# Performance work log

Hardware: AMD Instinct MI355X
Metric: run time of the kernel (lower is better)

The kernel has to match this reference:

```python
import jax, jax.numpy as jnp
import numpy as np

N_P, N_D = 100000, 50000
C, S, H = 128, 128, 128
E = 600000


def setup_inputs() -> dict:
    key = jax.random.key(0)
    ks = jax.random.split(key, 20)
    sc = 1.0 / np.sqrt(H)
    inp = {
        "h_p": jax.random.normal(ks[0], (N_P, C), dtype=jnp.float32),
        "h_d": jax.random.normal(ks[1], (N_D, S), dtype=jnp.float32),
        "pd_src": jax.random.randint(ks[2], (E,), 0, N_P),
        "pd_dst": jax.random.randint(ks[3], (E,), 0, N_D),
        "dp_src": jax.random.randint(ks[4], (E,), 0, N_D),
        "dp_dst": jax.random.randint(ks[5], (E,), 0, N_P),
    }
    names = [("W1_pd", (C, H)), ("W1_dp", (S, H)), ("W2_pd", (H, H)),
             ("W2_dp", (H, H)), ("W3_pd", (H, S)), ("W3_dp", (H, C))]
    for i, (nm, shp) in enumerate(names):
        inp[nm] = jax.random.normal(ks[6 + i], shp, dtype=jnp.float32) * sc
        inp["b" + nm[1:]] = jnp.zeros((shp[1],), dtype=jnp.float32)
    return inp


def gconv(x, src, dst, n_dst, W, b):
    """DGL GraphConv, norm='both': relu(D_dst^-1/2 A D_src^-1/2 X W + b)."""
    n_src = x.shape[0]
    ones = jnp.ones(src.shape, dtype=x.dtype)
    deg_out = jnp.maximum(jax.ops.segment_sum(ones, src, num_segments=n_src), 1.0)
    deg_in = jnp.maximum(jax.ops.segment_sum(ones, dst, num_segments=n_dst), 1.0)
    xs = x * jax.lax.rsqrt(deg_out)[:, None]
    m = jax.ops.segment_sum(xs[src], dst, num_segments=n_dst)  # [n_dst, d_in]
    m = m * jax.lax.rsqrt(deg_in)[:, None]
    return jax.nn.relu(m @ W + b)


def reference(h_p, h_d, pd_src, pd_dst, dp_src, dp_dst,
              W1_pd, b1_pd, W1_dp, b1_dp,
              W2_pd, b2_pd, W2_dp, b2_dp,
              W3_pd, b3_pd, W3_dp, b3_dp):
    # Layer 1: p_d sends p feats to d; d_p sends d feats to p
    h_d1 = gconv(h_p, pd_src, pd_dst, N_D, W1_pd, b1_pd)
    h_p1 = gconv(h_d, dp_src, dp_dst, N_P, W1_dp, b1_dp)
    # Layer 2
    h_d2 = gconv(h_p1, pd_src, pd_dst, N_D, W2_pd, b2_pd)
    h_p2 = gconv(h_d1, dp_src, dp_dst, N_P, W2_dp, b2_dp)
    # Layer 3: d gets S-dim, p gets C-dim
    h_d3 = gconv(h_p2, pd_src, pd_dst, N_D, W3_pd, b3_pd)
    h_p3 = gconv(h_d2, dp_src, dp_dst, N_P, W3_dp, b3_dp)
    return h_p3, h_d3
```

## Files before the change

kernel.cpp:

```cpp
#include <hip/hip_runtime.h>
#include <stdint.h>

#define N_P 100000
#define N_D 50000
#define NE  600000
#define F   128
#define FP  136

#define NCHK   16
#define CHKE   37504
#define HPH    4
#define HPS    8
#define HOFS_A0 ((size_t)0)
#define HOFS_A1 ((size_t)NCHK*N_P)
#define HOFS_A2 ((size_t)NCHK*N_P + (size_t)NCHK*N_D)
#define HOFS_A3 ((size_t)NCHK*N_P + (size_t)2*NCHK*N_D)

typedef __attribute__((ext_vector_type(8))) __bf16 bf16x8;
typedef __attribute__((ext_vector_type(4))) float  f32x4;

static __device__ __forceinline__ float bf2f(uint16_t u){
  union{float f;uint32_t i;} v; v.i = ((uint32_t)u)<<16; return v.f;
}
static __device__ __forceinline__ uint16_t f2bf(float f){
  union{float f;uint32_t i;} v; v.f = f;
  uint32_t i = v.i;
  uint32_t r = i + 0x7fffu + ((i>>16)&1u);
  return (uint16_t)(r>>16);
}

__global__ __launch_bounds__(512) void k_hist(
    const int* __restrict__ pd_src, const int* __restrict__ pd_dst,
    const int* __restrict__ dp_src, const int* __restrict__ dp_dst,
    int* __restrict__ hist){
  __shared__ uint32_t cnt[(N_P/HPH)/2];
  const int b = blockIdx.x;
  const int arr = b >> 6, part = (b >> 4) & 3, chunk = b & 15;
  const int* src; int N; size_t hofs;
  switch(arr){
    case 0:  src = pd_src; N = N_P; hofs = HOFS_A0; break;
    case 1:  src = pd_dst; N = N_D; hofs = HOFS_A1; break;
    case 2:  src = dp_src; N = N_D; hofs = HOFS_A2; break;
    default: src = dp_dst; N = N_P; hofs = HOFS_A3; break;
  }
  const int PART = N / HPH;
  const int nw   = PART >> 1;
  const int lo   = part * PART;
  for (int i = threadIdx.x; i < nw; i += 512) cnt[i] = 0;
  __syncthreads();
  const int e0 = chunk*CHKE, e1 = min(e0 + CHKE, NE);
  const uint4* s4 = (const uint4*)(src + e0);
  const int n4 = (e1 - e0) >> 2;
  for (int i = threadIdx.x; i < n4; i += 512){
    uint4 v = s4[i];
    int a0 = (int)v.x - lo, a1 = (int)v.y - lo, a2 = (int)v.z - lo, a3 = (int)v.w - lo;
    if ((unsigned)a0 < (unsigned)PART) atomicAdd(&cnt[a0>>1], 1u << ((a0&1)<<4));
    if ((unsigned)a1 < (unsigned)PART) atomicAdd(&cnt[a1>>1], 1u << ((a1&1)<<4));
    if ((unsigned)a2 < (unsigned)PART) atomicAdd(&cnt[a2>>1], 1u << ((a2&1)<<4));
    if ((unsigned)a3 < (unsigned)PART) atomicAdd(&cnt[a3>>1], 1u << ((a3&1)<<4));
  }
  __syncthreads();
  int* out = hist + hofs + (size_t)chunk*N + lo;
  for (int i = threadIdx.x; i < nw; i += 512){
    uint32_t w = cnt[i];
    out[2*i]   = (int)(w & 0xffffu);
    out[2*i+1] = (int)(w >> 16);
  }
}

__global__ void k_sumdeg(int* __restrict__ hist,
                         int* __restrict__ cnt_d_in, int* __restrict__ cnt_p_in,
                         float* __restrict__ rs_p_out, float* __restrict__ rs_p_in,
                         float* __restrict__ rs_d_out, float* __restrict__ rs_d_in){
  const int idx = blockIdx.x*256 + threadIdx.x;
  const int arr = blockIdx.y;
  int N; size_t hofs; bool pre;
  switch(arr){
    case 0:  N = N_P; hofs = HOFS_A0; pre = false; break;
    case 1:  N = N_D; hofs = HOFS_A1; pre = true;  break;
    case 2:  N = N_D; hofs = HOFS_A2; pre = false; break;
    default: N = N_P; hofs = HOFS_A3; pre = true;  break;
  }
  if (idx >= N) return;
  int* base = hist + hofs + idx;
  int run = 0;
  if (pre){
    #pragma unroll 4
    for (int c = 0; c < NCHK; ++c){
      int v = base[(size_t)c*N]; base[(size_t)c*N] = run; run += v;
    }
  } else {
    #pragma unroll 4
    for (int c = 0; c < NCHK; ++c) run += base[(size_t)c*N];
  }
  float rs = rsqrtf((float)max(run, 1));
  switch(arr){
    case 0:  rs_p_out[idx] = rs; break;
    case 1:  cnt_d_in[idx] = run; rs_d_in[idx] = rs; break;
    case 2:  rs_d_out[idx] = rs; break;
    default: cnt_p_in[idx] = run; rs_p_in[idx] = rs; break;
  }
}

__global__ void k_scan1(const int* __restrict__ cA, int nA,
                        const int* __restrict__ cB, int nB,
                        int* __restrict__ bsums, int nbA){
  __shared__ int red[8];
  int b = blockIdx.x, t = threadIdx.x;
  const int* in; int n, bi, slot;
  if (b < nbA){ in = cA; n = nA; bi = b;       slot = bi; }
  else        { in = cB; n = nB; bi = b - nbA; slot = 256 + bi; }
  int i = bi*512 + t;
  int v = (i < n) ? in[i] : 0;
  #pragma unroll
  for (int o = 32; o; o >>= 1) v += __shfl_down(v, o, 64);
  if ((t & 63) == 0) red[t >> 6] = v;
  __syncthreads();
  if (t == 0){ int s = 0; for (int k = 0; k < 8; ++k) s += red[k]; bsums[slot] = s; }
}

__global__ void k_scan2(int* bsums, int nbA, int nbB){
  __shared__ int sh[256];
  int seg = blockIdx.x, t = threadIdx.x;
  int nb = seg ? nbB : nbA;
  int* p = bsums + seg*256;
  int v = (t < nb) ? p[t] : 0;
  sh[t] = v; __syncthreads();
  for (int ofs = 1; ofs < 256; ofs <<= 1){
    int u = (t >= ofs) ? sh[t-ofs] : 0; __syncthreads();
    sh[t] += u; __syncthreads();
  }
  if (t < nb) p[t] = sh[t] - v;
}

__global__ void k_scan3(const int* __restrict__ cA, int nA,
                        const int* __restrict__ cB, int nB,
                        const int* __restrict__ bsums, int nbA,
                        int* __restrict__ offA, int* __restrict__ offB){
  __shared__ int sh[512];
  int b = blockIdx.x, t = threadIdx.x;
  const int* in; int n, bi; int* out; int base;
  if (b < nbA){ in = cA; n = nA; bi = b;       out = offA; base = bsums[bi]; }
  else        { in = cB; n = nB; bi = b - nbA; out = offB; base = bsums[256+bi]; }
  int i = bi*512 + t;
  int v = (i < n) ? in[i] : 0;
  sh[t] = v; __syncthreads();
  for (int ofs = 1; ofs < 512; ofs <<= 1){
    int u = (t >= ofs) ? sh[t-ofs] : 0; __syncthreads();
    sh[t] += u; __syncthreads();
  }
  if (i < n) out[i] = base + sh[t] - v;
  if (b == 0 && t == 0){ offA[nA] = NE; offB[nB] = NE; }
}

__global__ __launch_bounds__(512) void k_scatter(
    const int* __restrict__ pd_src, const int* __restrict__ pd_dst,
    const int* __restrict__ dp_src, const int* __restrict__ dp_dst,
    const int* __restrict__ off_pd, const int* __restrict__ off_dp,
    const int* __restrict__ hist,
    int* __restrict__ col_pd, int* __restrict__ col_dp){
  __shared__ int base[N_P/HPS];
  const int b = blockIdx.x;
  const int gph = b >> 7, part = (b >> 4) & 7, chunk = b & 15;
  const int* dsts; const int* srcs; const int* off; int* col; int N; size_t hofs;
  if (gph == 0){ dsts = pd_dst; srcs = pd_src; off = off_pd; col = col_pd; N = N_D; hofs = HOFS_A1; }
  else         { dsts = dp_dst; srcs = dp_src; off = off_dp; col = col_dp; N = N_P; hofs = HOFS_A3; }
  const int PART = N / HPS;
  const int lo = part * PART;
  const int* hc   = hist + hofs + (size_t)chunk*N + lo;
  const int* offp = off + lo;
  for (int i = threadIdx.x; i < PART; i += 512) base[i] = offp[i] + hc[i];
  __syncthreads();
  const int e0 = chunk*CHKE, e1 = min(e0 + CHKE, NE);
  const uint4* d4 = (const uint4*)(dsts + e0);
  const int n4 = (e1 - e0) >> 2;
  for (int i = threadIdx.x; i < n4; i += 512){
    uint4 d = d4[i];
    int a0 = (int)d.x - lo, a1 = (int)d.y - lo, a2 = (int)d.z - lo, a3 = (int)d.w - lo;
    int e = e0 + 4*i;
    if ((unsigned)a0 < (unsigned)PART){ int p = atomicAdd(&base[a0], 1); col[p] = srcs[e+0]; }
    if ((unsigned)a1 < (unsigned)PART){ int p = atomicAdd(&base[a1], 1); col[p] = srcs[e+1]; }
    if ((unsigned)a2 < (unsigned)PART){ int p = atomicAdd(&base[a2], 1); col[p] = srcs[e+2]; }
    if ((unsigned)a3 < (unsigned)PART){ int p = atomicAdd(&base[a3], 1); col[p] = srcs[e+3]; }
  }
}

__global__ void k_convert(const float4* __restrict__ hp, const float4* __restrict__ hd,
                          const float* __restrict__ rs_po, const float* __restrict__ rs_do,
                          uint2* __restrict__ P0, uint2* __restrict__ D0,
                          const float* w0,const float* w1,const float* w2,
                          const float* w3,const float* w4,const float* w5,
                          uint16_t* __restrict__ wt,
                          uint16_t* z0, uint16_t* z1, uint16_t* z2,
                          uint16_t* z3, uint16_t* z4, uint16_t* z5){
  if (blockIdx.x < 6){
    int m = blockIdx.x;
    const float* W; uint16_t* Z;
    switch(m){ case 0:W=w0;Z=z0;break; case 1:W=w1;Z=z1;break; case 2:W=w2;Z=z2;break;
               case 3:W=w3;Z=z3;break; case 4:W=w4;Z=z4;break; default:W=w5;Z=z5; }
    uint16_t* T = wt + m*F*FP;
    for (int idx = threadIdx.x; idx < F*F; idx += 256){
      int k = idx >> 7, j = idx & 127;
      T[j*FP + k] = f2bf(W[idx]);
    }
    if (threadIdx.x < F) Z[threadIdx.x] = 0;
    return;
  }
  int i = (blockIdx.x - 6)*256 + threadIdx.x;
  const int nP4 = N_P*F/4, nD4 = N_D*F/4;
  if (i < nP4){
    float4 v = hp[i]; float s = rs_po[i >> 5];
    uint2 r;
    r.x = ((uint32_t)f2bf(v.y*s)<<16) | f2bf(v.x*s);
    r.y = ((uint32_t)f2bf(v.w*s)<<16) | f2bf(v.z*s);
    P0[i] = r;
  } else {
    int j = i - nP4;
    if (j < nD4){
      float4 v = hd[j]; float s = rs_do[j >> 5];
      uint2 r;
      r.x = ((uint32_t)f2bf(v.y*s)<<16) | f2bf(v.x*s);
      r.y = ((uint32_t)f2bf(v.w*s)<<16) | f2bf(v.z*s);
      D0[j] = r;
    }
  }
}

template<int OUT_MODE>
__global__ __launch_bounds__(256, 4) void k_gconv2(
    const uint16_t* __restrict__ xA, const int* __restrict__ offAp, const int* __restrict__ colA,
    const float* __restrict__ rsA, const uint16_t* __restrict__ WtA, const float* __restrict__ biasA,
    const float* __restrict__ rsnA, void* __restrict__ outA, int ndA, int nsA, int nblkA,
    const uint16_t* __restrict__ xB, const int* __restrict__ offBp, const int* __restrict__ colB,
    const float* __restrict__ rsB, const uint16_t* __restrict__ WtB, const float* __restrict__ biasB,
    const float* __restrict__ rsnB, void* __restrict__ outB, int ndB, int nsB)
{
  __shared__ uint16_t m_lds[64*FP];
  const int tid  = threadIdx.x;
  const int lane = tid & 63;
  const int wv   = tid >> 6;

  const uint16_t* x; const int* off; const int* col; const float* rs_in;
  const uint16_t* Wt; const float* bias; const float* rs_next; void* outp;
  int n_dst, zrow, bid;
  if ((int)blockIdx.x < nblkA){
    x = xA; off = offAp; col = colA; rs_in = rsA; Wt = WtA; bias = biasA;
    rs_next = rsnA; outp = outA; n_dst = ndA; zrow = nsA; bid = blockIdx.x;
  } else {
    x = xB; off = offBp; col = colB; rs_in = rsB; Wt = WtB; bias = biasB;
    rs_next = rsnB; outp = outB; n_dst = ndB; zrow = nsB; bid = blockIdx.x - nblkA;
  }

  const int row0 = bid*64 + wv*16;
  const int g    = lane >> 4;
  const int l    = lane & 15;
  const uint16_t* xl = x + l*8;

  int e0a[4], e1a[4], cva[4];
  #pragma unroll
  for (int i = 0; i < 4; ++i){
    int r = row0 + i*4 + g;
    bool rv = r < n_dst;
    e0a[i] = rv ? off[r]   : 0;
    e1a[i] = rv ? off[r+1] : 0;
  }
  #pragma unroll
  for (int i = 0; i < 4; ++i){
    int last = (e1a[i] > 0) ? e1a[i]-1 : 0;
    int idx  = e0a[i] + l;
    cva[i] = col[idx < e1a[i] ? idx : last];
  }

  #pragma unroll
  for (int i = 0; i < 4; ++i){
    int e0 = e0a[i], e1 = e1a[i];
    int cv = cva[i];
    float a0=0.f,a1=0.f,a2=0.f,a3=0.f,a4=0.f,a5=0.f,a6=0.f,a7=0.f;
    for (int e = e0; e < e1; e += 16){
      int nidx = e + 16 + l;
      int ncv  = col[nidx < e1 ? nidx : e1-1];
      int cnt  = e1 - e;
      const bool more = (cnt > 8);
      int cb[16];
      #pragma unroll
      for (int q = 0; q < 8; ++q) cb[q] = __shfl(cv, g*16 + q, 64);
      if (more){
        #pragma unroll
        for (int q = 8; q < 16; ++q) cb[q] = __shfl(cv, g*16 + q, 64);
      }
      uint4 u[8], w[8];
      #pragma unroll
      for (int q = 0; q < 8; ++q){
        int c = (q < cnt) ? cb[q] : zrow;
        u[q] = *(const uint4*)(xl + (size_t)c*F);
      }
      if (more){
        #pragma unroll
        for (int q = 8; q < 16; ++q){
          int c = (q < cnt) ? cb[q] : zrow;
          w[q-8] = *(const uint4*)(xl + (size_t)c*F);
        }
      }
      #pragma unroll
      for (int q = 0; q < 8; ++q){
        a0 += bf2f((uint16_t)u[q].x); a1 += bf2f((uint16_t)(u[q].x>>16));
        a2 += bf2f((uint16_t)u[q].y); a3 += bf2f((uint16_t)(u[q].y>>16));
        a4 += bf2f((uint16_t)u[q].z); a5 += bf2f((uint16_t)(u[q].z>>16));
        a6 += bf2f((uint16_t)u[q].w); a7 += bf2f((uint16_t)(u[q].w>>16));
      }
      if (more){
        #pragma unroll
        for (int q = 0; q < 8; ++q){
          a0 += bf2f((uint16_t)w[q].x); a1 += bf2f((uint16_t)(w[q].x>>16));
          a2 += bf2f((uint16_t)w[q].y); a3 += bf2f((uint16_t)(w[q].y>>16));
          a4 += bf2f((uint16_t)w[q].z); a5 += bf2f((uint16_t)(w[q].z>>16));
          a6 += bf2f((uint16_t)w[q].w); a7 += bf2f((uint16_t)(w[q].w>>16));
        }
      }
      cv = ncv;
    }
    int r = row0 + i*4 + g;
    float rs = (r < n_dst) ? rs_in[r] : 0.f;
    uint4 pk;
    pk.x = ((uint32_t)f2bf(a1*rs)<<16) | f2bf(a0*rs);
    pk.y = ((uint32_t)f2bf(a3*rs)<<16) | f2bf(a2*rs);
    pk.z = ((uint32_t)f2bf(a5*rs)<<16) | f2bf(a4*rs);
    pk.w = ((uint32_t)f2bf(a7*rs)<<16) | f2bf(a6*rs);
    *(uint4*)&m_lds[(wv*16 + i*4 + g)*FP + l*8] = pk;
  }

  f32x4 acc[8];
  #pragma unroll
  for (int t = 0; t < 8; ++t) acc[t] = (f32x4){0.f,0.f,0.f,0.f};
  const int mrow = lane & 15;
  const int kgrp = lane >> 4;
  #pragma unroll
  for (int k0 = 0; k0 < F; k0 += 32){
    bf16x8 bfrag = *(const bf16x8*)&m_lds[(wv*16 + mrow)*FP + k0 + kgrp*8];
    #pragma unroll
    for (int t = 0; t < 8; ++t){
      bf16x8 afrag = *(const bf16x8*)&Wt[(t*16 + mrow)*FP + k0 + kgrp*8];
      acc[t] = __builtin_amdgcn_mfma_f32_16x16x32_bf16(afrag, bfrag, acc[t], 0, 0, 0);
    }
  }

  const int q4 = kgrp * 4;
  const int rr = row0 + mrow;
  if (rr < n_dst){
    float rsn = (OUT_MODE == 0) ? rs_next[rr] : 1.f;
    #pragma unroll
    for (int t = 0; t < 8; ++t){
      float4 b4 = *(const float4*)&bias[t*16 + q4];
      float v0 = fmaxf(acc[t][0] + b4.x, 0.f);
      float v1 = fmaxf(acc[t][1] + b4.y, 0.f);
      float v2 = fmaxf(acc[t][2] + b4.z, 0.f);
      float v3 = fmaxf(acc[t][3] + b4.w, 0.f);
      if (OUT_MODE == 0){
        uint2 pk;
        pk.x = ((uint32_t)f2bf(v1*rsn)<<16) | f2bf(v0*rsn);
        pk.y = ((uint32_t)f2bf(v3*rsn)<<16) | f2bf(v2*rsn);
        *(uint2*)((uint16_t*)outp + (size_t)rr*F + t*16 + q4) = pk;
      } else {
        float4 o; o.x = v0; o.y = v1; o.z = v2; o.w = v3;
        *(float4*)((float*)outp + (size_t)rr*F + t*16 + q4) = o;
      }
    }
  }
}

extern "C" void kernel_launch(void* const* d_in, const int* in_sizes, int n_in,
                              void* d_out, int out_size, void* d_ws, size_t ws_size,
                              hipStream_t stream) {
  const float* h_p   = (const float*)d_in[0];
  const float* h_d   = (const float*)d_in[1];
  const int* pd_src  = (const int*)d_in[2];
  const int* pd_dst  = (const int*)d_in[3];
  const int* dp_src  = (const int*)d_in[4];
  const int* dp_dst  = (const int*)d_in[5];
  const float* W1_pd = (const float*)d_in[6];   const float* b1_pd = (const float*)d_in[7];
  const float* W1_dp = (const float*)d_in[8];   const float* b1_dp = (const float*)d_in[9];
  const float* W2_pd = (const float*)d_in[10];  const float* b2_pd = (const float*)d_in[11];
  const float* W2_dp = (const float*)d_in[12];  const float* b2_dp = (const float*)d_in[13];
  const float* W3_pd = (const float*)d_in[14];  const float* b3_pd = (const float*)d_in[15];
  const float* W3_dp = (const float*)d_in[16];  const float* b3_dp = (const float*)d_in[17];

  char* w = (char*)d_ws;
  size_t o = 0;
  auto take = [&](size_t bytes)->char*{
    char* p = w + o; o += (bytes + 255) & ~(size_t)255; return p;
  };

  int* cnt_d_in  = (int*)take(4*(size_t)N_D);
  int* cnt_p_in  = (int*)take(4*(size_t)N_P);
  int* off_pd   = (int*)take(4*(size_t)(N_D+1));
  int* off_dp   = (int*)take(4*(size_t)(N_P+1));
  int* bsums    = (int*)take(4*512);
  int* col_pd   = (int*)take(4*(size_t)NE);
  int* col_dp   = (int*)take(4*(size_t)NE);
  float* rs_p_out = (float*)take(4*(size_t)N_P);
  float* rs_p_in  = (float*)take(4*(size_t)N_P);
  float* rs_d_out = (float*)take(4*(size_t)N_D);
  float* rs_d_in  = (float*)take(4*(size_t)N_D);
  uint16_t* wt  = (uint16_t*)take(2*(size_t)6*F*FP);
  uint16_t* P0  = (uint16_t*)take(2*(size_t)(N_P+1)*F);
  uint16_t* P1  = (uint16_t*)take(2*(size_t)(N_P+1)*F);
  uint16_t* P2  = (uint16_t*)take(2*(size_t)(N_P+1)*F);
  uint16_t* D0  = (uint16_t*)take(2*(size_t)(N_D+1)*F);
  uint16_t* D1  = (uint16_t*)take(2*(size_t)(N_D+1)*F);
  uint16_t* D2  = (uint16_t*)take(2*(size_t)(N_D+1)*F);

  int* hist = (int*)P1;

  k_hist<<<4*HPH*NCHK, 512, 0, stream>>>(pd_src, pd_dst, dp_src, dp_dst, hist);
  k_sumdeg<<<dim3((N_P+255)/256, 4), 256, 0, stream>>>(
      hist, cnt_d_in, cnt_p_in, rs_p_out, rs_p_in, rs_d_out, rs_d_in);
  const int nbA = (N_D + 511)/512;
  const int nbB = (N_P + 511)/512;
  k_scan1<<<nbA+nbB, 512, 0, stream>>>(cnt_d_in, N_D, cnt_p_in, N_P, bsums, nbA);
  k_scan2<<<2, 256, 0, stream>>>(bsums, nbA, nbB);
  k_scan3<<<nbA+nbB, 512, 0, stream>>>(cnt_d_in, N_D, cnt_p_in, N_P, bsums, nbA, off_pd, off_dp);
  k_scatter<<<2*HPS*NCHK, 512, 0, stream>>>(pd_src, pd_dst, dp_src, dp_dst,
                                            off_pd, off_dp, hist, col_pd, col_dp);
  k_convert<<<((N_P+N_D)*F/4 + 255)/256 + 6, 256, 0, stream>>>(
      (const float4*)h_p, (const float4*)h_d, rs_p_out, rs_d_out, (uint2*)P0, (uint2*)D0,
      W1_pd, W1_dp, W2_pd, W2_dp, W3_pd, W3_dp, wt,
      P0 + (size_t)N_P*F, D0 + (size_t)N_D*F,
      P1 + (size_t)N_P*F, D1 + (size_t)N_D*F,
      P2 + (size_t)N_P*F, D2 + (size_t)N_D*F);

  const int gd = (N_D + 63)/64, gp = (N_P + 63)/64;
  k_gconv2<0><<<gd+gp, 256, 0, stream>>>(
      P0, off_pd, col_pd, rs_d_in, wt + 0*F*FP, b1_pd, rs_d_out, D1, N_D, N_P, gd,
      D0, off_dp, col_dp, rs_p_in, wt + 1*F*FP, b1_dp, rs_p_out, P1, N_P, N_D);
  k_gconv2<0><<<gd+gp, 256, 0, stream>>>(
      P1, off_pd, col_pd, rs_d_in, wt + 2*F*FP, b2_pd, rs_d_out, D2, N_D, N_P, gd,
      D1, off_dp, col_dp, rs_p_in, wt + 3*F*FP, b2_dp, rs_p_out, P2, N_P, N_D);
  k_gconv2<1><<<gd+gp, 256, 0, stream>>>(
      P2, off_pd, col_pd, rs_d_in, wt + 4*F*FP, b3_pd, nullptr, (float*)d_out + (size_t)N_P*F, N_D, N_P, gd,
      D2, off_dp, col_dp, rs_p_in, wt + 5*F*FP, b3_dp, nullptr, (float*)d_out, N_P, N_D);
}
```

Baseline: 446.9 us.

## Fuse CSR build and feature conversion into one cooperative kernel with grid syncs

Replaces the seven preprocessing launches (histogram, degree sum, three-phase scan, scatter, convert) with a single cooperative kernel of 256 blocks that separates the phases with grid.sync(). The feature/weight conversion work is spread into the phases that are otherwise underutilised, such as the scan stages, so it overlaps with them. Launch gaps and tail idle time between the small kernels are meant to be removed. The gather loads in the aggregation kernel also switch to nontemporal loads. Risks: grid-sync cost, a fixed grid of 256 blocks for the histogram and scatter phases, and a fallback path if the cooperative launch fails.

```diff
diff --git a/kernel.cpp b/kernel.cpp
--- a/kernel.cpp
+++ b/kernel.cpp
@@ -1,5 +1,8 @@
 #include <hip/hip_runtime.h>
+#include <hip/hip_cooperative_groups.h>
 #include <stdint.h>
+
+namespace cg = cooperative_groups;
 
 #define N_P 100000
 #define N_D 50000
@@ -11,13 +14,20 @@
 #define CHKE   37504
 #define HPH    4
 #define HPS    8
+#define NBLD   256
+#define NBA    ((N_D + 511)/512)
+#define NBB    ((N_P + 511)/512)
 #define HOFS_A0 ((size_t)0)
 #define HOFS_A1 ((size_t)NCHK*N_P)
 #define HOFS_A2 ((size_t)NCHK*N_P + (size_t)NCHK*N_D)
 #define HOFS_A3 ((size_t)NCHK*N_P + (size_t)2*NCHK*N_D)
+#define CVT_TOT (6 + (N_P+N_D)*F/4/256)
+#define CVT_A   6252
+#define CVT_B   12504
 
 typedef __attribute__((ext_vector_type(8))) __bf16 bf16x8;
 typedef __attribute__((ext_vector_type(4))) float  f32x4;
+typedef unsigned int __attribute__((ext_vector_type(4))) u32x4;
 
 static __device__ __forceinline__ float bf2f(uint16_t u){
   union{float f;uint32_t i;} v; v.i = ((uint32_t)u)<<16; return v.f;
@@ -27,6 +37,256 @@
   uint32_t i = v.i;
   uint32_t r = i + 0x7fffu + ((i>>16)&1u);
   return (uint16_t)(r>>16);
+}
+static __device__ __forceinline__ uint4 ld_nt_u4(const uint16_t* p){
+  u32x4 v = __builtin_nontemporal_load((const u32x4*)p);
+  uint4 r; r.x = v.x; r.y = v.y; r.z = v.z; r.w = v.w; return r;
+}
+
+static __device__ __forceinline__ void convert_ob(
+    int ob, int t,
+    const float4* __restrict__ hp, const float4* __restrict__ hd,
+    const float* __restrict__ rs_po, const float* __restrict__ rs_do,
+    uint2* __restrict__ P0, uint2* __restrict__ D0,
+    const float* w0,const float* w1,const float* w2,
+    const float* w3,const float* w4,const float* w5,
+    uint16_t* __restrict__ wt,
+    uint16_t* z0, uint16_t* z1, uint16_t* z2,
+    uint16_t* z3, uint16_t* z4, uint16_t* z5)
+{
+  if (ob < 6){
+    const float* W; uint16_t* Z;
+    switch(ob){ case 0:W=w0;Z=z0;break; case 1:W=w1;Z=z1;break; case 2:W=w2;Z=z2;break;
+                case 3:W=w3;Z=z3;break; case 4:W=w4;Z=z4;break; default:W=w5;Z=z5; }
+    uint16_t* T = wt + ob*F*FP;
+    for (int idx = t; idx < F*F; idx += 256){
+      int k = idx >> 7, j = idx & 127;
+      T[j*FP + k] = f2bf(W[idx]);
+    }
+    if (t < F) Z[t] = 0;
+    return;
+  }
+  int i = (ob - 6)*256 + t;
+  const int nP4 = N_P*F/4, nD4 = N_D*F/4;
+  if (i < nP4){
+    float4 v = hp[i]; float s = rs_po[i >> 5];
+    uint2 r;
+    r.x = ((uint32_t)f2bf(v.y*s)<<16) | f2bf(v.x*s);
+    r.y = ((uint32_t)f2bf(v.w*s)<<16) | f2bf(v.z*s);
+    P0[i] = r;
+  } else {
+    int j = i - nP4;
+    if (j < nD4){
+      float4 v = hd[j]; float s = rs_do[j >> 5];
+      uint2 r;
+      r.x = ((uint32_t)f2bf(v.y*s)<<16) | f2bf(v.x*s);
+      r.y = ((uint32_t)f2bf(v.w*s)<<16) | f2bf(v.z*s);
+      D0[j] = r;
+    }
+  }
+}
+
+__global__ __launch_bounds__(512) void k_build(
+    const int* __restrict__ pd_src, const int* __restrict__ pd_dst,
+    const int* __restrict__ dp_src, const int* __restrict__ dp_dst,
+    int* __restrict__ hist,
+    int* __restrict__ cnt_d_in, int* __restrict__ cnt_p_in,
+    float* __restrict__ rs_p_out, float* __restrict__ rs_p_in,
+    float* __restrict__ rs_d_out, float* __restrict__ rs_d_in,
+    int* __restrict__ bsums,
+    int* __restrict__ off_pd, int* __restrict__ off_dp,
+    int* __restrict__ col_pd, int* __restrict__ col_dp,
+    const float4* __restrict__ hp, const float4* __restrict__ hd,
+    uint2* __restrict__ P0, uint2* __restrict__ D0,
+    const float* w0,const float* w1,const float* w2,
+    const float* w3,const float* w4,const float* w5,
+    uint16_t* __restrict__ wt,
+    uint16_t* z0, uint16_t* z1, uint16_t* z2,
+    uint16_t* z3, uint16_t* z4, uint16_t* z5)
+{
+  __shared__ union {
+    uint32_t cnt[(N_P/HPH)/2];
+    int      base[N_P/HPS];
+    int      sh512[512];
+    int      sh256[256];
+  } sm;
+  __shared__ int red2[8];
+  cg::grid_group grid = cg::this_grid();
+  const int t = threadIdx.x;
+  const int b = blockIdx.x;
+
+  {
+    const int arr = b >> 6, part = (b >> 4) & 3, chunk = b & 15;
+    const int* src; int N; size_t hofs;
+    switch(arr){
+      case 0:  src = pd_src; N = N_P; hofs = HOFS_A0; break;
+      case 1:  src = pd_dst; N = N_D; hofs = HOFS_A1; break;
+      case 2:  src = dp_src; N = N_D; hofs = HOFS_A2; break;
+      default: src = dp_dst; N = N_P; hofs = HOFS_A3; break;
+    }
+    const int PART = N / HPH;
+    const int nw   = PART >> 1;
+    const int lo   = part * PART;
+    for (int i = t; i < nw; i += 512) sm.cnt[i] = 0;
+    __syncthreads();
+    const int e0 = chunk*CHKE, e1 = min(e0 + CHKE, NE);
+    const uint4* s4 = (const uint4*)(src + e0);
+    const int n4 = (e1 - e0) >> 2;
+    for (int i = t; i < n4; i += 512){
+      uint4 v = s4[i];
+      int a0 = (int)v.x - lo, a1 = (int)v.y - lo, a2 = (int)v.z - lo, a3 = (int)v.w - lo;
+      if ((unsigned)a0 < (unsigned)PART) atomicAdd(&sm.cnt[a0>>1], 1u << ((a0&1)<<4));
+      if ((unsigned)a1 < (unsigned)PART) atomicAdd(&sm.cnt[a1>>1], 1u << ((a1&1)<<4));
+      if ((unsigned)a2 < (unsigned)PART) atomicAdd(&sm.cnt[a2>>1], 1u << ((a2&1)<<4));
+      if ((unsigned)a3 < (unsigned)PART) atomicAdd(&sm.cnt[a3>>1], 1u << ((a3&1)<<4));
+    }
+    __syncthreads();
+    int* out = hist + hofs + (size_t)chunk*N + lo;
+    for (int i = t; i < nw; i += 512){
+      uint32_t wv = sm.cnt[i];
+      out[2*i]   = (int)(wv & 0xffffu);
+      out[2*i+1] = (int)(wv >> 16);
+    }
+  }
+  grid.sync();
+
+  {
+    const int gtid = b*512 + t;
+    const int T0 = N_P, T1 = N_P+N_D, T2 = N_P+2*N_D, T3 = 2*N_P+2*N_D;
+    for (int w = gtid; w < T3; w += NBLD*512){
+      int arr, idx;
+      if      (w < T0){ arr = 0; idx = w; }
+      else if (w < T1){ arr = 1; idx = w - T0; }
+      else if (w < T2){ arr = 2; idx = w - T1; }
+      else            { arr = 3; idx = w - T2; }
+      int N; size_t hofs; bool pre;
+      switch(arr){
+        case 0:  N = N_P; hofs = HOFS_A0; pre = false; break;
+        case 1:  N = N_D; hofs = HOFS_A1; pre = true;  break;
+        case 2:  N = N_D; hofs = HOFS_A2; pre = false; break;
+        default: N = N_P; hofs = HOFS_A3; pre = true;  break;
+      }
+      int* basep = hist + hofs + idx;
+      int run = 0;
+      if (pre){
+        #pragma unroll 4
+        for (int c = 0; c < NCHK; ++c){
+          int v = basep[(size_t)c*N]; basep[(size_t)c*N] = run; run += v;
+        }
+      } else {
+        #pragma unroll 4
+        for (int c = 0; c < NCHK; ++c) run += basep[(size_t)c*N];
+      }
+      float rs = rsqrtf((float)max(run, 1));
+      switch(arr){
+        case 0:  rs_p_out[idx] = rs; break;
+        case 1:  cnt_d_in[idx] = run; rs_d_in[idx] = rs; break;
+        case 2:  rs_d_out[idx] = rs; break;
+        default: cnt_p_in[idx] = run; rs_p_in[idx] = rs; break;
+      }
+    }
+  }
+  grid.sync();
+
+  {
+    for (int tb = b; tb < NBA+NBB; tb += NBLD){
+      const int* in; int n, bi, slot;
+      if (tb < NBA){ in = cnt_d_in; n = N_D; bi = tb;       slot = bi; }
+      else         { in = cnt_p_in; n = N_P; bi = tb - NBA; slot = 256 + bi; }
+      int i = bi*512 + t;
+      int v = (i < n) ? in[i] : 0;
+      #pragma unroll
+      for (int o = 32; o; o >>= 1) v += __shfl_down(v, o, 64);
+      if ((t & 63) == 0) red2[t >> 6] = v;
+      __syncthreads();
+      if (t == 0){ int s = 0; for (int k = 0; k < 8; ++k) s += red2[k]; bsums[slot] = s; }
+      __syncthreads();
+    }
+    for (int p0 = 0 + b*2; p0 < CVT_A; p0 += NBLD*2){
+      int ob = p0 + (t >> 8);
+      if (ob < CVT_A)
+        convert_ob(ob, t & 255, hp, hd, rs_p_out, rs_d_out, P0, D0,
+                   w0,w1,w2,w3,w4,w5, wt, z0,z1,z2,z3,z4,z5);
+    }
+  }
+  grid.sync();
+
+  if (b == 0){
+    for (int seg = 0; seg < 2; ++seg){
+      int nb = seg ? NBB : NBA;
+      int* p = bsums + seg*256;
+      int v = 0;
+      if (t < 256){ v = (t < nb) ? p[t] : 0; sm.sh256[t] = v; }
+      __syncthreads();
+      for (int ofs = 1; ofs < 256; ofs <<= 1){
+        int u2 = 0;
+        if (t < 256 && t >= ofs) u2 = sm.sh256[t-ofs];
+        __syncthreads();
+        if (t < 256) sm.sh256[t] += u2;
+        __syncthreads();
+      }
+      if (t < nb) p[t] = sm.sh256[t] - v;
+      __syncthreads();
+    }
+  } else {
+    for (int p0 = CVT_A + (b-1)*2; p0 < CVT_B; p0 += (NBLD-1)*2){
+      int ob = p0 + (t >> 8);
+      if (ob < CVT_B)
+        convert_ob(ob, t & 255, hp, hd, rs_p_out, rs_d_out, P0, D0,
+                   w0,w1,w2,w3,w4,w5, wt, z0,z1,z2,z3,z4,z5);
+    }
+  }
+  grid.sync();
+
+  {
+    for (int tb = b; tb < NBA+NBB; tb += NBLD){
+      const int* in; int n, bi; int* outp; int base;
+      if (tb < NBA){ in = cnt_d_in; n = N_D; bi = tb;       outp = off_pd; base = bsums[bi]; }
+      else         { in = cnt_p_in; n = N_P; bi = tb - NBA; outp = off_dp; base = bsums[256+bi]; }
+      int i = bi*512 + t;
+      int v = (i < n) ? in[i] : 0;
+      sm.sh512[t] = v; __syncthreads();
+      for (int ofs = 1; ofs < 512; ofs <<= 1){
+        int u2 = (t >= ofs) ? sm.sh512[t-ofs] : 0; __syncthreads();
+        sm.sh512[t] += u2; __syncthreads();
+      }
+      if (i < n) outp[i] = base + sm.sh512[t] - v;
+      __syncthreads();
+    }
+    if (b == 0 && t == 0){ off_pd[N_D] = NE; off_dp[N_P] = NE; }
+    for (int p0 = CVT_B + b*2; p0 < CVT_TOT; p0 += NBLD*2){
+      int ob = p0 + (t >> 8);
+      if (ob < CVT_TOT)
+        convert_ob(ob, t & 255, hp, hd, rs_p_out, rs_d_out, P0, D0,
+                   w0,w1,w2,w3,w4,w5, wt, z0,z1,z2,z3,z4,z5);
+    }
+  }
+  grid.sync();
+
+  {
+    const int gph = b >> 7, part = (b >> 4) & 7, chunk = b & 15;
+    const int* dsts; const int* srcs; const int* off; int* col; int N; size_t hofs;
+    if (gph == 0){ dsts = pd_dst; srcs = pd_src; off = off_pd; col = col_pd; N = N_D; hofs = HOFS_A1; }
+    else         { dsts = dp_dst; srcs = dp_src; off = off_dp; col = col_dp; N = N_P; hofs = HOFS_A3; }
+    const int PART = N / HPS;
+    const int lo = part * PART;
+    const int* hc   = hist + hofs + (size_t)chunk*N + lo;
+    const int* offp = off + lo;
+    for (int i = t; i < PART; i += 512) sm.base[i] = offp[i] + hc[i];
+    __syncthreads();
+    const int e0 = chunk*CHKE, e1 = min(e0 + CHKE, NE);
+    const uint4* d4 = (const uint4*)(dsts + e0);
+    const int n4 = (e1 - e0) >> 2;
+    for (int i = t; i < n4; i += 512){
+      uint4 d = d4[i];
+      int a0 = (int)d.x - lo, a1 = (int)d.y - lo, a2 = (int)d.z - lo, a3 = (int)d.w - lo;
+      int e = e0 + 4*i;
+      if ((unsigned)a0 < (unsigned)PART){ int p = atomicAdd(&sm.base[a0], 1); col[p] = srcs[e+0]; }
+      if ((unsigned)a1 < (unsigned)PART){ int p = atomicAdd(&sm.base[a1], 1); col[p] = srcs[e+1]; }
+      if ((unsigned)a2 < (unsigned)PART){ int p = atomicAdd(&sm.base[a2], 1); col[p] = srcs[e+2]; }
+      if ((unsigned)a3 < (unsigned)PART){ int p = atomicAdd(&sm.base[a3], 1); col[p] = srcs[e+3]; }
+    }
+  }
 }
 
 __global__ __launch_bounds__(512) void k_hist(
@@ -193,37 +453,8 @@
                           uint16_t* __restrict__ wt,
                           uint16_t* z0, uint16_t* z1, uint16_t* z2,
                           uint16_t* z3, uint16_t* z4, uint16_t* z5){
-  if (blockIdx.x < 6){
-    int m = blockIdx.x;
-    const float* W; uint16_t* Z;
-    switch(m){ case 0:W=w0;Z=z0;break; case 1:W=w1;Z=z1;break; case 2:W=w2;Z=z2;break;
-               case 3:W=w3;Z=z3;break; case 4:W=w4;Z=z4;break; default:W=w5;Z=z5; }
-    uint16_t* T = wt + m*F*FP;
-    for (int idx = threadIdx.x; idx < F*F; idx += 256){
-      int k = idx >> 7, j = idx & 127;
-      T[j*FP + k] = f2bf(W[idx]);
-    }
-    if (threadIdx.x < F) Z[threadIdx.x] = 0;
-    return;
-  }
-  int i = (blockIdx.x - 6)*256 + threadIdx.x;
-  const int nP4 = N_P*F/4, nD4 = N_D*F/4;
-  if (i < nP4){
-    float4 v = hp[i]; float s = rs_po[i >> 5];
-    uint2 r;
-    r.x = ((uint32_t)f2bf(v.y*s)<<16) | f2bf(v.x*s);
-    r.y = ((uint32_t)f2bf(v.w*s)<<16) | f2bf(v.z*s);
-    P0[i] = r;
-  } else {
-    int j = i - nP4;
-    if (j < nD4){
-      float4 v = hd[j]; float s = rs_do[j >> 5];
-      uint2 r;
-      r.x = ((uint32_t)f2bf(v.y*s)<<16) | f2bf(v.x*s);
-      r.y = ((uint32_t)f2bf(v.w*s)<<16) | f2bf(v.z*s);
-      D0[j] = r;
-    }
-  }
+  convert_ob(blockIdx.x, threadIdx.x, hp, hd, rs_po, rs_do, P0, D0,
+             w0,w1,w2,w3,w4,w5, wt, z0,z1,z2,z3,z4,z5);
 }
 
 template<int OUT_MODE>
@@ -292,13 +523,13 @@
       #pragma unroll
       for (int q = 0; q < 8; ++q){
         int c = (q < cnt) ? cb[q] : zrow;
-        u[q] = *(const uint4*)(xl + (size_t)c*F);
+        u[q] = ld_nt_u4(xl + (size_t)c*F);
       }
       if (more){
         #pragma unroll
         for (int q = 8; q < 16; ++q){
           int c = (q < cnt) ? cb[q] : zrow;
-          w[q-8] = *(const uint4*)(xl + (size_t)c*F);
+          w[q-8] = ld_nt_u4(xl + (size_t)c*F);
         }
       }
       #pragma unroll
@@ -411,22 +642,44 @@
 
   int* hist = (int*)P1;
 
-  k_hist<<<4*HPH*NCHK, 512, 0, stream>>>(pd_src, pd_dst, dp_src, dp_dst, hist);
-  k_sumdeg<<<dim3((N_P+255)/256, 4), 256, 0, stream>>>(
-      hist, cnt_d_in, cnt_p_in, rs_p_out, rs_p_in, rs_d_out, rs_d_in);
-  const int nbA = (N_D + 511)/512;
-  const int nbB = (N_P + 511)/512;
-  k_scan1<<<nbA+nbB, 512, 0, stream>>>(cnt_d_in, N_D, cnt_p_in, N_P, bsums, nbA);
-  k_scan2<<<2, 256, 0, stream>>>(bsums, nbA, nbB);
-  k_scan3<<<nbA+nbB, 512, 0, stream>>>(cnt_d_in, N_D, cnt_p_in, N_P, bsums, nbA, off_pd, off_dp);
-  k_scatter<<<2*HPS*NCHK, 512, 0, stream>>>(pd_src, pd_dst, dp_src, dp_dst,
-                                            off_pd, off_dp, hist, col_pd, col_dp);
-  k_convert<<<((N_P+N_D)*F/4 + 255)/256 + 6, 256, 0, stream>>>(
-      (const float4*)h_p, (const float4*)h_d, rs_p_out, rs_d_out, (uint2*)P0, (uint2*)D0,
-      W1_pd, W1_dp, W2_pd, W2_dp, W3_pd, W3_dp, wt,
-      P0 + (size_t)N_P*F, D0 + (size_t)N_D*F,
-      P1 + (size_t)N_P*F, D1 + (size_t)N_D*F,
-      P2 + (size_t)N_P*F, D2 + (size_t)N_D*F);
+  const float4* hp4 = (const float4*)h_p;
+  const float4* hd4 = (const float4*)h_d;
+  uint2* P0u = (uint2*)P0;
+  uint2* D0u = (uint2*)D0;
+  uint16_t* z0 = P0 + (size_t)N_P*F;
+  uint16_t* z1 = D0 + (size_t)N_D*F;
+  uint16_t* z2 = P1 + (size_t)N_P*F;
+  uint16_t* z3 = D1 + (size_t)N_D*F;
+  uint16_t* z4 = P2 + (size_t)N_P*F;
+  uint16_t* z5 = D2 + (size_t)N_D*F;
+
+  void* kargs[] = {
+    (void*)&pd_src, (void*)&pd_dst, (void*)&dp_src, (void*)&dp_dst,
+    (void*)&hist, (void*)&cnt_d_in, (void*)&cnt_p_in,
+    (void*)&rs_p_out, (void*)&rs_p_in, (void*)&rs_d_out, (void*)&rs_d_in,
+    (void*)&bsums, (void*)&off_pd, (void*)&off_dp, (void*)&col_pd, (void*)&col_dp,
+    (void*)&hp4, (void*)&hd4, (void*)&P0u, (void*)&D0u,
+    (void*)&W1_pd, (void*)&W1_dp, (void*)&W2_pd, (void*)&W2_dp, (void*)&W3_pd, (void*)&W3_dp,
+    (void*)&wt,
+    (void*)&z0, (void*)&z1, (void*)&z2, (void*)&z3, (void*)&z4, (void*)&z5
+  };
+  hipError_t cerr = hipLaunchCooperativeKernel(reinterpret_cast<void*>(k_build),
+                                               dim3(NBLD), dim3(512), kargs, 0, stream);
+  if (cerr != hipSuccess){
+    const int nbA = NBA, nbB = NBB;
+    k_hist<<<4*HPH*NCHK, 512, 0, stream>>>(pd_src, pd_dst, dp_src, dp_dst, hist);
+    k_sumdeg<<<dim3((N_P+255)/256, 4), 256, 0, stream>>>(
+        hist, cnt_d_in, cnt_p_in, rs_p_out, rs_p_in, rs_d_out, rs_d_in);
+    k_scan1<<<nbA+nbB, 512, 0, stream>>>(cnt_d_in, N_D, cnt_p_in, N_P, bsums, nbA);
+    k_scan2<<<2, 256, 0, stream>>>(bsums, nbA, nbB);
+    k_scan3<<<nbA+nbB, 512, 0, stream>>>(cnt_d_in, N_D, cnt_p_in, N_P, bsums, nbA, off_pd, off_dp);
+    k_scatter<<<2*HPS*NCHK, 512, 0, stream>>>(pd_src, pd_dst, dp_src, dp_dst,
+                                              off_pd, off_dp, hist, col_pd, col_dp);
+    k_convert<<<CVT_TOT, 256, 0, stream>>>(
+        hp4, hd4, rs_p_out, rs_d_out, P0u, D0u,
+        W1_pd, W1_dp, W2_pd, W2_dp, W3_pd, W3_dp, wt,
+        z0, z1, z2, z3, z4, z5);
+  }
 
   const int gd = (N_D + 63)/64, gp = (N_P + 63)/64;
   k_gconv2<0><<<gd+gp, 256, 0, stream>>>(
```

After: 743.1 us. +66.3%, slower.
